# Kernel optimization log

Hardware: AMD Instinct MI355X
Metric: run time of the kernel (lower is better)

Reference implementation:

```python
import jax, jax.numpy as jnp
import numpy as np
import math

NPAD = 100      # npadding
NLAYERS = 4     # transformer_num_layers
NHEAD = 8       # transformer_nhead


def _posenc(T, d):
    pos = jnp.arange(T, dtype=jnp.float32)[:, None]
    div = jnp.exp(jnp.arange(0, d, 2, dtype=jnp.float32) * (-(math.log(1000.0) / d)))
    pe = jnp.zeros((T, d), jnp.float32)
    pe = pe.at[:, 0::2].set(jnp.sin(pos * div))
    pe = pe.at[:, 1::2].set(jnp.cos(pos * div))
    return pe


def _ln(x, g, b):
    m = x.mean(-1, keepdims=True)
    v = ((x - m) ** 2).mean(-1, keepdims=True)
    return (x - m) / jnp.sqrt(v + 1e-5) * g + b


def conv_individual(Y, kernel, npadding):
    # Y: (B,N,Ttot); kernel: (ntau,N). Causal zero-pad then FFT conv (faithful to source).
    B, N, Ttot = Y.shape
    kernel = jnp.concatenate([jnp.zeros((1, N), kernel.dtype), kernel], axis=0)
    ntau = kernel.shape[0]
    nn = Ttot + ntau - 1
    Yf = jnp.fft.fft(Y, n=nn, axis=2)                 # (B,N,nn) complex
    Kf = jnp.fft.fft(kernel.T, n=nn, axis=-1)          # (N,nn)
    c = jnp.fft.ifft(Yf * Kf[None], axis=2).real
    c = jnp.where(jnp.abs(c) < 1e-5, 0.0, c)           # ad-hoc small-value zeroing from source
    return c[:, :, :Ttot][:, :, npadding:]             # (B,N,T)


def conv_subspace(Y, kernel, npadding):
    # Y: (B,N,Ttot); kernel: (ntau,S) -> G: (B,N,S,T)
    B, N, Ttot = Y.shape
    k = kernel[None]                                   # (1,ntau,S)
    k = jnp.concatenate([jnp.zeros((1, 1, k.shape[2]), jnp.float32), k], axis=1)
    ntau = k.shape[1]
    nn = Ttot + ntau - 1
    Yf = jnp.fft.fft(Y, n=nn, axis=2)[..., None]       # (B,N,nn,1)
    Kf = jnp.fft.fft(k, n=nn, axis=1)[None]            # (1,1,nn,S)
    G = jnp.fft.ifft(Yf * Kf, axis=2).real             # (B,N,nn,S)
    G = jnp.where(jnp.abs(G) < 1e-5, 0.0, G)
    G = G[:, :, :Ttot, :][:, :, npadding:, :]
    return jnp.swapaxes(G, -1, -2)                     # (B,N,S,T)


def _encoder(x, Wqkv, bqkv, Wo, bo, ln1_g, ln1_b, W1, b1, W2, b2, ln2_g, ln2_b):
    B, T, D = x.shape
    hd = D // NHEAD
    for l in range(NLAYERS):
        qkv = x @ Wqkv[l] + bqkv[l]                    # (B,T,3D)
        q, k, v = jnp.split(qkv, 3, axis=-1)
        q = q.reshape(B, T, NHEAD, hd)
        k = k.reshape(B, T, NHEAD, hd)
        v = v.reshape(B, T, NHEAD, hd)
        scores = jnp.einsum('bthd,bshd->bhts', q, k) / jnp.sqrt(jnp.float32(hd))
        attn = jax.nn.softmax(scores, axis=-1)
        o = jnp.einsum('bhts,bshd->bthd', attn, v).reshape(B, T, D)
        x = _ln(x + (o @ Wo[l] + bo[l]), ln1_g[l], ln1_b[l])
        ff = jax.nn.gelu(x @ W1[l] + b1[l], approximate=False) @ W2[l] + b2[l]
        x = _ln(x + ff, ln2_g[l], ln2_b[l])
    return x


def reference(Y, token_W, token_b, Wqkv, bqkv, Wo, bo, ln1_g, ln1_b, W1, b1, W2, b2,
              ln2_g, ln2_b, toL_W, toL_b, dec_W1, dec_b1, dec_W2, dec_b2,
              stimulus_basis, readout_W, coupling_W, coupling_basis, self_kernel):
    B, N, Ttot = Y.shape
    T = Ttot - NPAD
    D = token_W.shape[1]
    # token conversion over time (seq dim = time)
    x = jnp.swapaxes(Y[:, :, NPAD:], 1, 2) @ token_W + token_b   # (B,T,D)
    x = x + _posenc(T, D)[None]
    x = _encoder(x, Wqkv, bqkv, Wo, bo, ln1_g, ln1_b, W1, b1, W2, b2, ln2_g, ln2_b)
    pooled = x.mean(axis=1)                                      # (B,D)
    h = pooled @ toL_W + toL_b                                   # (B,2Z)
    Z = h.shape[1] // 2
    z = h[:, :Z]                                                 # mu (sample_latent=False)
    # stimulus decoder (2-layer MLP)
    coeffs = jax.nn.relu(z @ dec_W1 + dec_b1) @ dec_W2 + dec_b2  # (B, NF*NB)
    NB = stimulus_basis.shape[1]
    NF = coeffs.shape[1] // NB
    coeffs = coeffs.reshape(B, NF, NB)
    sti_lat = jnp.einsum('bfk,tk->bft', coeffs, stimulus_basis)  # (B,NF,T)
    sti = jnp.einsum('nf,bft->bnt', readout_W, sti_lat)          # (B,N,T)
    # coupling via FFT causal conv into subspaces
    G = conv_subspace(Y, coupling_basis, NPAD)                   # (B,N,S,T)
    cpl = jnp.einsum('ns,bnst->bnt', coupling_W, G)
    # self-history FFT causal conv
    slf = conv_individual(Y, self_kernel, NPAD)
    return sti + cpl + slf                                       # log firing rate (B,N,T)


def setup_inputs() -> dict:
    key = jax.random.key(0)
    ks = jax.random.split(key, 30)
    B, N, Ttot = 16, 256, 1100
    D, FF, Zdim = 256, 1024, 64
    NB, NF, S, NTAU = 30, 4, 4, 20   # NF = narea*stimulus_nfactor = 2*2
    T = Ttot - NPAD
    sc = 0.02
    inp = {
        'Y': jax.random.uniform(ks[0], (B, N, Ttot), jnp.float32),
        'token_W': jax.random.normal(ks[1], (N, D), jnp.float32) * sc,
        'token_b': jnp.zeros((D,), jnp.float32),
        'Wqkv': jax.random.normal(ks[2], (NLAYERS, D, 3 * D), jnp.float32) * sc,
        'bqkv': jnp.zeros((NLAYERS, 3 * D), jnp.float32),
        'Wo': jax.random.normal(ks[3], (NLAYERS, D, D), jnp.float32) * sc,
        'bo': jnp.zeros((NLAYERS, D), jnp.float32),
        'ln1_g': jnp.ones((NLAYERS, D), jnp.float32),
        'ln1_b': jnp.zeros((NLAYERS, D), jnp.float32),
        'W1': jax.random.normal(ks[4], (NLAYERS, D, FF), jnp.float32) * sc,
        'b1': jnp.zeros((NLAYERS, FF), jnp.float32),
        'W2': jax.random.normal(ks[5], (NLAYERS, FF, D), jnp.float32) * sc,
        'b2': jnp.zeros((NLAYERS, D), jnp.float32),
        'ln2_g': jnp.ones((NLAYERS, D), jnp.float32),
        'ln2_b': jnp.zeros((NLAYERS, D), jnp.float32),
        'toL_W': jax.random.normal(ks[6], (D, 2 * Zdim), jnp.float32) * sc,
        'toL_b': jnp.zeros((2 * Zdim,), jnp.float32),
        'dec_W1': jax.random.normal(ks[7], (Zdim, 2 * Zdim), jnp.float32) * sc,
        'dec_b1': jnp.zeros((2 * Zdim,), jnp.float32),
        'dec_W2': jax.random.normal(ks[8], (2 * Zdim, NB * NF), jnp.float32) * sc * 0.001,
        'dec_b2': jnp.zeros((NB * NF,), jnp.float32),
        'stimulus_basis': jax.random.normal(ks[9], (T, NB), jnp.float32),
        'readout_W': jax.random.normal(ks[10], (N, NF), jnp.float32) * sc,
        'coupling_W': jax.random.normal(ks[11], (N, S), jnp.float32) * sc,
        'coupling_basis': jax.random.normal(ks[12], (NTAU, S), jnp.float32) * 0.1,
        'self_kernel': jax.random.normal(ks[13], (NTAU, N), jnp.float32) * 0.1,
    }
    return inp
```

## Files before the change

kernel.cpp:

```cpp
#include <hip/hip_runtime.h>
#include <math.h>

#define TT_   1000
#define TTOT_ 1100
#define NPAD_ 100
#define DD_   256
#define NN_   256

#define X_OFF    0u
#define XB_OFF   4096000u
#define O_OFF    6144000u
#define BIG_OFF  12288000u
#define WT_OFF   20480000u
#define PE_OFF   22085632u
#define PP_OFF   22341632u
#define PL_OFF   (PP_OFF + 32768u)
#define CF_OFF   (PL_OFF + 4096u)
#define CB_OFF   (CF_OFF + 1920u)
#define BQ_OFF   (CB_OFF + 5120u)
#define STL_OFF  (BQ_OFF + 3072u)

#define SC2_ 0.25503902254649546f

typedef __attribute__((ext_vector_type(8))) short s16x8;
typedef __attribute__((ext_vector_type(4))) float f32x4;
typedef __attribute__((ext_vector_type(16))) float f32x16;
typedef __attribute__((ext_vector_type(4))) unsigned u32x4;

__device__ inline short f2bf(float f) {
    unsigned u = __float_as_uint(f);
    u += 0x7fffu + ((u >> 16) & 1u);
    return (short)(u >> 16);
}
__device__ inline float exp2i(float x) {
    float r; asm("v_exp_f32 %0, %1" : "=v"(r) : "v"(x)); return r;
}

__device__ inline void gl_lds16(const short* g, short* l) {
    __builtin_amdgcn_global_load_lds(
        (const __attribute__((address_space(1))) void*)g,
        (__attribute__((address_space(3))) void*)l, 16, 0, 0);
}

__global__ __launch_bounds__(256) void wtr_k(const float* __restrict__ in,
                                             short* __restrict__ out, int K, int N,
                                             int qrows, float qs)
{
    __shared__ float t[32][33];
    const int n0 = blockIdx.x * 32, k0 = blockIdx.y * 32;
    in  += (size_t)blockIdx.z * K * N;
    out += (size_t)blockIdx.z * K * N;
    const int tx = threadIdx.x & 31, ty = threadIdx.x >> 5;
    #pragma unroll
    for (int i = 0; i < 4; ++i)
        t[ty + 8 * i][tx] = in[(size_t)(k0 + ty + 8 * i) * N + n0 + tx];
    __syncthreads();
    #pragma unroll
    for (int i = 0; i < 4; ++i) {
        const int row = n0 + ty + 8 * i;
        float f = t[tx][ty + 8 * i];
        if (row < qrows) f *= qs;
        out[(size_t)row * K + k0 + tx] = f2bf(f);
    }
}

__global__ __launch_bounds__(256) void ytr_k(const float* __restrict__ Y,
                                             short* __restrict__ out)
{
    __shared__ float t[32][33];
    const int b = blockIdx.z;
    const int t0 = blockIdx.x * 32, n0 = blockIdx.y * 32;
    const int tx = threadIdx.x & 31, ty = threadIdx.x >> 5;
    #pragma unroll
    for (int i = 0; i < 4; ++i) {
        const int tt = t0 + tx;
        t[ty + 8 * i][tx] = (tt < TT_)
            ? Y[((size_t)(b * NN_ + n0 + ty + 8 * i)) * TTOT_ + NPAD_ + tt] : 0.f;
    }
    __syncthreads();
    #pragma unroll
    for (int i = 0; i < 4; ++i) {
        const int tt = t0 + ty + 8 * i;
        if (tt < TT_)
            out[((size_t)(b * TT_ + tt)) * NN_ + n0 + tx] = f2bf(t[tx][ty + 8 * i]);
    }
}

__global__ void pe_k(float* __restrict__ PE)
{
    const int t = blockIdx.x, d = threadIdx.x;
    const float div = __expf(-(float)(d & ~1) * 0.0269834190585241f);
    const float ang = (float)t * div;
    PE[t * 256 + d] = (d & 1) ? cosf(ang) : sinf(ang);
}

__global__ void bscale_k(const float* __restrict__ in, float* __restrict__ out)
{
    const int i = blockIdx.x * 256 + threadIdx.x;
    if (i < 3072) {
        const int col = i % 768;
        out[i] = in[i] * ((col < 256) ? SC2_ : 1.f);
    }
}

template<int OUTBF, int ACT, int RES, int DUAL>
__global__ __launch_bounds__(256) void bgemm_k(const short* __restrict__ A,
                                               const short* __restrict__ Bt,
                                               const float* __restrict__ bias,
                                               const float* __restrict__ resid,
                                               void* __restrict__ Cout,
                                               short* __restrict__ Cb,
                                               int M, int N, int K, int nby)
{
    __shared__ short As[64 * 64];
    __shared__ short Bs[128 * 64];
    const int tid = threadIdx.x;

    const int nwg = gridDim.x;
    int gid = blockIdx.x;
    {
        const int q = nwg >> 3, r = nwg & 7;
        const int x = gid & 7, idx = gid >> 3;
        gid = (x < r ? x * (q + 1) : r * (q + 1) + (x - r) * q) + idx;
    }
    const int bx = gid / nby, by = gid - bx * nby;
    const int m0 = bx * 64, n0 = by * 128;

    const int wv = tid >> 6, lane = tid & 63;
    const int wr = wv >> 1, wc = wv & 1;
    const int l15 = lane & 15, lg = lane >> 4;

    f32x4 acc[2][4];
    #pragma unroll
    for (int i = 0; i < 2; ++i)
        #pragma unroll
        for (int j = 0; j < 4; ++j) acc[i][j] = (f32x4){0.f, 0.f, 0.f, 0.f};

    const int nt = K >> 6;
    for (int t = 0; t < nt; ++t) {
        __syncthreads();
        const int k0 = t << 6;
        #pragma unroll
        for (int i = 0; i < 2; ++i) {
            const int cid = i * 256 + tid;
            const int r = cid >> 3, c = cid & 7;
            gl_lds16(A + (size_t)(m0 + r) * K + k0 + ((c ^ (r & 7)) * 8), As + cid * 8);
        }
        #pragma unroll
        for (int i = 0; i < 4; ++i) {
            const int cid = i * 256 + tid;
            const int r = cid >> 3, c = cid & 7;
            gl_lds16(Bt + (size_t)(n0 + r) * K + k0 + ((c ^ (r & 7)) * 8), Bs + cid * 8);
        }
        __syncthreads();

        #pragma unroll
        for (int ks = 0; ks < 2; ++ks) {
            s16x8 af[2], bf[4];
            #pragma unroll
            for (int mi = 0; mi < 2; ++mi) {
                const int row = wr * 32 + mi * 16 + l15;
                const int ch = ks * 4 + lg;
                af[mi] = *(const s16x8*)(As + row * 64 + ((ch ^ (row & 7)) * 8));
            }
            #pragma unroll
            for (int ni = 0; ni < 4; ++ni) {
                const int col = wc * 64 + ni * 16 + l15;
                const int ch = ks * 4 + lg;
                bf[ni] = *(const s16x8*)(Bs + col * 64 + ((ch ^ (col & 7)) * 8));
            }
            #pragma unroll
            for (int mi = 0; mi < 2; ++mi)
                #pragma unroll
                for (int ni = 0; ni < 4; ++ni)
                    acc[mi][ni] = __builtin_amdgcn_mfma_f32_16x16x32_bf16(
                        af[mi], bf[ni], acc[mi][ni], 0, 0, 0);
        }
    }

    #pragma unroll
    for (int mi = 0; mi < 2; ++mi) {
        #pragma unroll
        for (int ni = 0; ni < 4; ++ni) {
            const int col = n0 + wc * 64 + ni * 16 + l15;
            const float bv = bias[col];
            #pragma unroll
            for (int r = 0; r < 4; ++r) {
                const int row = m0 + wr * 32 + mi * 16 + lg * 4 + r;
                float v = acc[mi][ni][r] + bv;
                if (RES == 1) v += resid[(size_t)row * N + col];
                if (RES == 2) v += resid[(size_t)(row % 1000) * N + col];
                if (ACT) v = 0.5f * v * (1.0f + erff(v * 0.70710678118654752f));
                if (OUTBF) ((short*)Cout)[(size_t)row * N + col] = f2bf(v);
                else       ((float*)Cout)[(size_t)row * N + col] = v;
                if (DUAL)  Cb[(size_t)row * N + col] = f2bf(v);
            }
        }
    }
}

__global__ __launch_bounds__(512) void bgemmln_k(const short* __restrict__ A,
                                                 const short* __restrict__ Bt,
                                                 const float* __restrict__ bias,
                                                 const float* __restrict__ lng,
                                                 const float* __restrict__ lnb,
                                                 float* __restrict__ X,
                                                 short* __restrict__ Xb,
                                                 int K)
{
    __shared__ short As[64 * 64];
    __shared__ short Bs[256 * 64];
    __shared__ float red[64][4][2];
    __shared__ float mrs[64][2];
    const int tid = threadIdx.x;

    const int nwg = gridDim.x;
    int gid = blockIdx.x;
    {
        const int q = nwg >> 3, r = nwg & 7;
        const int x = gid & 7, idx = gid >> 3;
        gid = (x < r ? x * (q + 1) : r * (q + 1) + (x - r) * q) + idx;
    }
    const int m0 = gid * 64;

    const int wv = tid >> 6, lane = tid & 63;
    const int wr = wv >> 2, wcx = wv & 3;
    const int l15 = lane & 15, lg = lane >> 4;

    f32x4 acc[2][4];
    #pragma unroll
    for (int i = 0; i < 2; ++i)
        #pragma unroll
        for (int j = 0; j < 4; ++j) acc[i][j] = (f32x4){0.f, 0.f, 0.f, 0.f};

    const int nt = K >> 6;
    for (int t = 0; t < nt; ++t) {
        __syncthreads();
        const int k0 = t << 6;
        {
            const int r = tid >> 3, c = tid & 7;
            gl_lds16(A + (size_t)(m0 + r) * K + k0 + ((c ^ (r & 7)) * 8), As + tid * 8);
        }
        #pragma unroll
        for (int i = 0; i < 4; ++i) {
            const int cid = i * 512 + tid;
            const int r = cid >> 3, c = cid & 7;
            gl_lds16(Bt + (size_t)r * K + k0 + ((c ^ (r & 7)) * 8), Bs + cid * 8);
        }
        __syncthreads();

        #pragma unroll
        for (int ks = 0; ks < 2; ++ks) {
            s16x8 af[2], bf[4];
            #pragma unroll
            for (int mi = 0; mi < 2; ++mi) {
                const int row = wr * 32 + mi * 16 + l15;
                const int ch = ks * 4 + lg;
                af[mi] = *(const s16x8*)(As + row * 64 + ((ch ^ (row & 7)) * 8));
            }
            #pragma unroll
            for (int ni = 0; ni < 4; ++ni) {
                const int col = wcx * 64 + ni * 16 + l15;
                const int ch = ks * 4 + lg;
                bf[ni] = *(const s16x8*)(Bs + col * 64 + ((ch ^ (col & 7)) * 8));
            }
            #pragma unroll
            for (int mi = 0; mi < 2; ++mi)
                #pragma unroll
                for (int ni = 0; ni < 4; ++ni)
                    acc[mi][ni] = __builtin_amdgcn_mfma_f32_16x16x32_bf16(
                        af[mi], bf[ni], acc[mi][ni], 0, 0, 0);
        }
    }

    float v[2][4][4];
    #pragma unroll
    for (int mi = 0; mi < 2; ++mi)
        #pragma unroll
        for (int ni = 0; ni < 4; ++ni) {
            const int col = wcx * 64 + ni * 16 + l15;
            const float bv = bias[col];
            #pragma unroll
            for (int r = 0; r < 4; ++r) {
                const int row = m0 + wr * 32 + mi * 16 + lg * 4 + r;
                v[mi][ni][r] = acc[mi][ni][r] + bv + X[(size_t)row * 256 + col];
            }
        }

    #pragma unroll
    for (int mi = 0; mi < 2; ++mi)
        #pragma unroll
        for (int r = 0; r < 4; ++r) {
            float ss = v[mi][0][r] + v[mi][1][r] + v[mi][2][r] + v[mi][3][r];
            float qq = v[mi][0][r] * v[mi][0][r] + v[mi][1][r] * v[mi][1][r]
                     + v[mi][2][r] * v[mi][2][r] + v[mi][3][r] * v[mi][3][r];
            #pragma unroll
            for (int msk = 1; msk < 16; msk <<= 1) {
                ss += __shfl_xor(ss, msk);
                qq += __shfl_xor(qq, msk);
            }
            if (l15 == 0) {
                const int rloc = wr * 32 + mi * 16 + lg * 4 + r;
                red[rloc][wcx][0] = ss;
                red[rloc][wcx][1] = qq;
            }
        }
    __syncthreads();
    if (tid < 64) {
        const float s = red[tid][0][0] + red[tid][1][0] + red[tid][2][0] + red[tid][3][0];
        const float q = red[tid][0][1] + red[tid][1][1] + red[tid][2][1] + red[tid][3][1];
        const float mean = s * (1.f / 256.f);
        const float var = q * (1.f / 256.f) - mean * mean;
        mrs[tid][0] = mean;
        mrs[tid][1] = rsqrtf(var + 1e-5f);
    }
    __syncthreads();

    #pragma unroll
    for (int mi = 0; mi < 2; ++mi)
        #pragma unroll
        for (int ni = 0; ni < 4; ++ni) {
            const int col = wcx * 64 + ni * 16 + l15;
            const float gg = lng[col], bb = lnb[col];
            #pragma unroll
            for (int r = 0; r < 4; ++r) {
                const int rloc = wr * 32 + mi * 16 + lg * 4 + r;
                const int row = m0 + rloc;
                const float o = (v[mi][ni][r] - mrs[rloc][0]) * mrs[rloc][1] * gg + bb;
                X[(size_t)row * 256 + col] = o;
                Xb[(size_t)row * 256 + col] = f2bf(o);
            }
        }
}

__global__ __launch_bounds__(512) void mattn_k(const short* __restrict__ qkv,
                                               short* __restrict__ o)
{
    int wg = blockIdx.x;
    wg = (wg & 7) * 64 + (wg >> 3);
    const int qt = wg & 3, h = (wg >> 2) & 7, b = wg >> 5;

    const int tid = threadIdx.x, wv = tid >> 6, lane = tid & 63;
    const int q31 = lane & 31, hi = lane >> 5;
    __shared__ short Ks[2][64 * 40];
    __shared__ short VT[2][32 * 72];

    const int q0w = qt * 256 + wv * 32;
    int qrow = q0w + q31; if (qrow > 999) qrow = 999;
    s16x8 bq[2];
    #pragma unroll
    for (int dh = 0; dh < 2; ++dh)
        bq[dh] = *(const s16x8*)(qkv + ((size_t)(b * TT_ + qrow)) * 768 + h * 32 + dh * 16 + hi * 8);

    f32x16 oacc;
    #pragma unroll
    for (int i = 0; i < 16; ++i) oacc[i] = 0.f;
    float lrun = 0.f;

    const int sr = tid >> 2, sc = tid & 3;
    const int u = tid & 255;
    const int kp = u >> 3, dq = (u & 7) * 4;
    s16x8 kreg;
    short4 va, vb;
    auto LOADT = [&](int kt) {
        if (tid < 256) {
            int t = kt * 64 + sr; if (t > 999) t = 999;
            kreg = *(const s16x8*)(qkv + ((size_t)(b * TT_ + t)) * 768 + 256 + h * 32 + sc * 8);
        } else {
            int t0 = kt * 64 + 2 * kp, t1 = t0 + 1;
            if (t0 > 999) t0 = 999;
            if (t1 > 999) t1 = 999;
            va = *(const short4*)(qkv + ((size_t)(b * TT_ + t0)) * 768 + 512 + h * 32 + dq);
            vb = *(const short4*)(qkv + ((size_t)(b * TT_ + t1)) * 768 + 512 + h * 32 + dq);
        }
    };
    auto WRITET = [&](int buf) {
        if (tid < 256) {
            *(s16x8*)(&Ks[buf][sr * 40 + sc * 8]) = kreg;
        } else {
            const int c = kp >> 2;
            const int ko = (2 * kp) & 7;
            const uint2 vaw = *(const uint2*)&va;
            const uint2 vbw = *(const uint2*)&vb;
            unsigned pk[4];
            pk[0] = __builtin_amdgcn_perm(vbw.x, vaw.x, 0x05040100u);
            pk[1] = __builtin_amdgcn_perm(vbw.x, vaw.x, 0x07060302u);
            pk[2] = __builtin_amdgcn_perm(vbw.y, vaw.y, 0x05040100u);
            pk[3] = __builtin_amdgcn_perm(vbw.y, vaw.y, 0x07060302u);
            #pragma unroll
            for (int j = 0; j < 4; ++j) {
                const int d = dq + j;
                *(unsigned*)(&VT[buf][d * 72 + ((c ^ (d >> 3)) * 8) + ko]) = pk[j];
            }
        }
    };

    LOADT(0); WRITET(0);
    __syncthreads();
    int cur = 0;

    for (int kt = 0; kt < 16; ++kt) {
        if (kt < 15) LOADT(kt + 1);

        f32x16 st[2];
        __builtin_amdgcn_s_setprio(1);
        #pragma unroll
        for (int kb = 0; kb < 2; ++kb) {
            s16x8 kf0 = *(const s16x8*)(&Ks[cur][(kb * 32 + q31) * 40 + hi * 8]);
            s16x8 kf1 = *(const s16x8*)(&Ks[cur][(kb * 32 + q31) * 40 + 16 + hi * 8]);
            f32x16 z;
            #pragma unroll
            for (int i = 0; i < 16; ++i) z[i] = 0.f;
            z = __builtin_amdgcn_mfma_f32_32x32x16_bf16(kf0, bq[0], z, 0, 0, 0);
            z = __builtin_amdgcn_mfma_f32_32x32x16_bf16(kf1, bq[1], z, 0, 0, 0);
            st[kb] = z;
        }
        __builtin_amdgcn_s_setprio(0);

        if (kt == 15) {
            #pragma unroll
            for (int kb = 0; kb < 2; ++kb)
                #pragma unroll
                for (int r = 0; r < 16; ++r) {
                    const int kloc = kb * 32 + (r & 3) + 8 * (r >> 2) + 4 * hi;
                    if (960 + kloc >= TT_) st[kb][r] = -1e30f;
                }
        }

        float sloc = 0.f;
        #pragma unroll
        for (int kb = 0; kb < 2; ++kb)
            #pragma unroll
            for (int r = 0; r < 16; ++r) {
                const float p = exp2i(st[kb][r]);
                st[kb][r] = p; sloc += p;
            }
        lrun += sloc;

        unsigned wk[2][4][2];
        #pragma unroll
        for (int kb = 0; kb < 2; ++kb)
            #pragma unroll
            for (int a = 0; a < 4; ++a)
                #pragma unroll
                for (int h2 = 0; h2 < 2; ++h2) {
                    unsigned rr;
                    asm("v_cvt_pk_bf16_f32 %0, %1, %2"
                        : "=v"(rr)
                        : "v"(st[kb][4 * a + 2 * h2]), "v"(st[kb][4 * a + 2 * h2 + 1]));
                    wk[kb][a][h2] = rr;
                }

        #pragma unroll
        for (int ks = 0; ks < 4; ++ks) {
            const int kb = ks >> 1, qq = ks & 1;
            unsigned X0 = wk[kb][2 * qq + 1][0], Y0 = wk[kb][2 * qq][0];
            unsigned X1 = wk[kb][2 * qq + 1][1], Y1 = wk[kb][2 * qq][1];
            asm("v_permlane32_swap_b32 %0, %1" : "+v"(X0), "+v"(Y0));
            asm("v_permlane32_swap_b32 %0, %1" : "+v"(X1), "+v"(Y1));
            u32x4 w4 = (u32x4){Y0, Y1, X0, X1};
            s16x8 pb = __builtin_bit_cast(s16x8, w4);
            s16x8 vf = *(const s16x8*)(&VT[cur][q31 * 72 + (((2 * ks + hi) ^ (q31 >> 3)) * 8)]);
            __builtin_amdgcn_s_setprio(1);
            oacc = __builtin_amdgcn_mfma_f32_32x32x16_bf16(vf, pb, oacc, 0, 0, 0);
            __builtin_amdgcn_s_setprio(0);
        }

        if (kt < 15) WRITET(cur ^ 1);
        __syncthreads();
        cur ^= 1;
    }

    lrun += __shfl_xor(lrun, 32);

    const int t = q0w + q31;
    if (t < TT_) {
        const float inv = 1.f / lrun;
        short* ob = o + ((size_t)(b * TT_ + t)) * 256 + h * 32;
        #pragma unroll
        for (int a = 0; a < 4; ++a) {
            unsigned w0, w1;
            asm("v_cvt_pk_bf16_f32 %0, %1, %2"
                : "=v"(w0) : "v"(oacc[4 * a + 0] * inv), "v"(oacc[4 * a + 1] * inv));
            asm("v_cvt_pk_bf16_f32 %0, %1, %2"
                : "=v"(w1) : "v"(oacc[4 * a + 2] * inv), "v"(oacc[4 * a + 3] * inv));
            const int d0 = 8 * a + 4 * hi;
            *(unsigned*)(ob + d0) = w0;
            *(unsigned*)(ob + d0 + 2) = w1;
        }
    }
}

__global__ __launch_bounds__(256) void pool_part_k(const float* __restrict__ X,
                                                   float* __restrict__ partial)
{
    const int b = blockIdx.x, seg = blockIdx.y, d = threadIdx.x;
    float s = 0.f;
    const int t0 = seg * 125;
    for (int t = t0; t < t0 + 125; ++t) s += X[((size_t)b * TT_ + t) * 256 + d];
    partial[(b * 8 + seg) * 256 + d] = s;
}
__global__ __launch_bounds__(256) void pool_red_k(const float* __restrict__ partial,
                                                  float* __restrict__ pooled)
{
    const int b = blockIdx.x, d = threadIdx.x;
    float s = 0.f;
    for (int k = 0; k < 8; ++k) s += partial[(b * 8 + k) * 256 + d];
    pooled[b * 256 + d] = s * (1.f / (float)TT_);
}

__global__ __launch_bounds__(128) void head_k(const float* __restrict__ pooled,
                                              const float* __restrict__ toLW,
                                              const float* __restrict__ toLb,
                                              const float* __restrict__ dW1,
                                              const float* __restrict__ db1,
                                              const float* __restrict__ dW2,
                                              const float* __restrict__ db2,
                                              float* __restrict__ coeffs)
{
    const int b = blockIdx.x, j = threadIdx.x;
    __shared__ float hs[64];
    __shared__ float hid[128];
    float a = toLb[j];
    for (int d = 0; d < 256; ++d) a += pooled[b * 256 + d] * toLW[d * 128 + j];
    if (j < 64) hs[j] = a;
    __syncthreads();
    float a2 = db1[j];
    for (int z = 0; z < 64; ++z) a2 += hs[z] * dW1[z * 128 + j];
    hid[j] = fmaxf(a2, 0.f);
    __syncthreads();
    if (j < 120) {
        float a3 = db2[j];
        for (int k = 0; k < 128; ++k) a3 += hid[k] * dW2[k * 120 + j];
        coeffs[b * 120 + j] = a3;
    }
}

__global__ void comb_k(const float* __restrict__ selfK,
                       const float* __restrict__ cplW,
                       const float* __restrict__ cplB,
                       float* __restrict__ comb)
{
    const int n = threadIdx.x;
    for (int ti = 0; ti < 20; ++ti) {
        float s = selfK[ti * 256 + n];
        #pragma unroll
        for (int si = 0; si < 4; ++si) s += cplW[n * 4 + si] * cplB[ti * 4 + si];
        comb[n * 20 + ti] = s;
    }
}

__global__ __launch_bounds__(256) void stilat_k(const float* __restrict__ SB,
                                                const float* __restrict__ coeffs,
                                                float* __restrict__ STL)
{
    const int bf = blockIdx.x;
    __shared__ float c[30];
    if (threadIdx.x < 30) c[threadIdx.x] = coeffs[(bf >> 2) * 120 + (bf & 3) * 30 + threadIdx.x];
    __syncthreads();
    for (int t = threadIdx.x; t < TT_; t += 256) {
        float acc = 0.f;
        const float* sp = SB + (size_t)t * 30;
        #pragma unroll
        for (int k = 0; k < 30; ++k) acc += c[k] * sp[k];
        STL[bf * TT_ + t] = acc;
    }
}

__global__ __launch_bounds__(256) void final_k(const float* __restrict__ Y,
                                               const float* __restrict__ STL,
                                               const float* __restrict__ roW,
                                               const float* __restrict__ comb,
                                               float* __restrict__ out)
{
    const int bx = blockIdx.x;
    const int ts = bx & 3, nc = (bx >> 2) & 31, b = bx >> 7;
    const int n0 = nc * 8, t0 = ts * 250;
    const int tid = threadIdx.x;
    __shared__ float rw[8][4], ck[8][20], yl[8][272];

    if (tid < 32) rw[tid >> 2][tid & 3] = roW[(n0 + (tid >> 2)) * 4 + (tid & 3)];
    if (tid >= 64 && tid < 224) {
        const int j = tid - 64;
        ck[j / 20][j % 20] = comb[(n0 + j / 20) * 20 + (j % 20)];
    }
    for (int j = tid; j < 2160; j += 256) {
        const int n = j / 270, jj = j - n * 270;
        yl[n][jj] = Y[((size_t)(b * 256 + n0 + n)) * TTOT_ + t0 + 80 + jj];
    }
    __syncthreads();

    if (tid < 250) {
        const int t = t0 + tid;
        float s4[4];
        #pragma unroll
        for (int f = 0; f < 4; ++f) s4[f] = STL[((size_t)b * 4 + f) * TT_ + t];
        #pragma unroll
        for (int n = 0; n < 8; ++n) {
            float acc = rw[n][0] * s4[0] + rw[n][1] * s4[1]
                      + rw[n][2] * s4[2] + rw[n][3] * s4[3];
            #pragma unroll
            for (int tau = 1; tau <= 20; ++tau)
                acc += ck[n][tau - 1] * yl[n][tid + 20 - tau];
            out[((size_t)(b * 256 + n0 + n)) * TT_ + t] = acc;
        }
    }
}

extern "C" void kernel_launch(void* const* d_in, const int* in_sizes, int n_in,
                              void* d_out, int out_size, void* d_ws, size_t ws_size,
                              hipStream_t stream)
{
    const float* Y      = (const float*)d_in[0];
    const float* tokW   = (const float*)d_in[1];
    const float* tokb   = (const float*)d_in[2];
    const float* Wqkv   = (const float*)d_in[3];
    const float* bqkv   = (const float*)d_in[4];
    const float* Wo     = (const float*)d_in[5];
    const float* bo     = (const float*)d_in[6];
    const float* ln1g   = (const float*)d_in[7];
    const float* ln1b   = (const float*)d_in[8];
    const float* W1     = (const float*)d_in[9];
    const float* b1     = (const float*)d_in[10];
    const float* W2     = (const float*)d_in[11];
    const float* b2     = (const float*)d_in[12];
    const float* ln2g   = (const float*)d_in[13];
    const float* ln2b   = (const float*)d_in[14];
    const float* toLW   = (const float*)d_in[15];
    const float* toLb   = (const float*)d_in[16];
    const float* dW1    = (const float*)d_in[17];
    const float* db1    = (const float*)d_in[18];
    const float* dW2    = (const float*)d_in[19];
    const float* db2    = (const float*)d_in[20];
    const float* SB     = (const float*)d_in[21];
    const float* roW    = (const float*)d_in[22];
    const float* cplW   = (const float*)d_in[23];
    const float* cplB   = (const float*)d_in[24];
    const float* selfK  = (const float*)d_in[25];

    float* ws  = (float*)d_ws;
    float* X   = ws + X_OFF;
    short* Xb  = (short*)(ws + XB_OFF);
    short* O   = (short*)(ws + O_OFF);
    short* BIG = (short*)(ws + BIG_OFF);
    short* WT  = (short*)(ws + WT_OFF);
    float* PE  = ws + PE_OFF;
    float* PP  = ws + PP_OFF;
    float* PL  = ws + PL_OFF;
    float* CF  = ws + CF_OFF;
    float* CB  = ws + CB_OFF;
    float* BQ  = ws + BQ_OFF;
    float* STL = ws + STL_OFF;

    short* WTqkv = WT;
    short* WTo   = WT + 786432;
    short* WTw1  = WT + 1048576;
    short* WTw2  = WT + 2097152;
    short* WTtok = WT + 3145728;
    short* Ybt   = BIG;

    wtr_k<<<dim3(24, 8, 4), 256, 0, stream>>>(Wqkv, WTqkv, 256, 768, 256, SC2_);
    wtr_k<<<dim3(8, 8, 4),  256, 0, stream>>>(Wo,   WTo,   256, 256, 0, 1.f);
    wtr_k<<<dim3(32, 8, 4), 256, 0, stream>>>(W1,   WTw1,  256, 1024, 0, 1.f);
    wtr_k<<<dim3(8, 32, 4), 256, 0, stream>>>(W2,   WTw2,  1024, 256, 0, 1.f);
    wtr_k<<<dim3(8, 8, 1),  256, 0, stream>>>(tokW, WTtok, 256, 256, 0, 1.f);
    bscale_k<<<12, 256, 0, stream>>>(bqkv, BQ);
    pe_k<<<1000, 256, 0, stream>>>(PE);
    ytr_k<<<dim3(32, 8, 16), 256, 0, stream>>>(Y, Ybt);

    bgemm_k<0, 0, 2, 1><<<500, 256, 0, stream>>>(
        Ybt, WTtok, tokb, PE, X, Xb, 16000, 256, 256, 2);

    for (int l = 0; l < 4; ++l) {
        bgemm_k<1, 0, 0, 0><<<1500, 256, 0, stream>>>(
            Xb, WTqkv + (size_t)l * 196608, BQ + l * 768, nullptr, BIG, nullptr,
            16000, 768, 256, 6);
        mattn_k<<<512, 512, 0, stream>>>(BIG, O);
        bgemmln_k<<<250, 512, 0, stream>>>(
            O, WTo + (size_t)l * 65536, bo + l * 256,
            ln1g + l * 256, ln1b + l * 256, X, Xb, 256);
        bgemm_k<1, 1, 0, 0><<<2000, 256, 0, stream>>>(
            Xb, WTw1 + (size_t)l * 262144, b1 + l * 1024, nullptr, BIG, nullptr,
            16000, 1024, 256, 8);
        bgemmln_k<<<250, 512, 0, stream>>>(
            BIG, WTw2 + (size_t)l * 262144, b2 + l * 256,
            ln2g + l * 256, ln2b + l * 256, X, Xb, 1024);
    }

    pool_part_k<<<dim3(16, 8), 256, 0, stream>>>(X, PP);
    pool_red_k<<<16, 256, 0, stream>>>(PP, PL);
    head_k<<<16, 128, 0, stream>>>(PL, toLW, toLb, dW1, db1, dW2, db2, CF);
    comb_k<<<1, 256, 0, stream>>>(selfK, cplW, cplB, CB);
    stilat_k<<<64, 256, 0, stream>>>(SB, CF, STL);
    final_k<<<2048, 256, 0, stream>>>(Y, STL, roW, CB, (float*)d_out);
}
```

Baseline: 497.3 us.

## Double-buffer QKV/FFN1 GEMM loads and halve LN-GEMM row tile for occupancy

Adds a GEMM kernel that prefetches the next K-tile into a second LDS buffer while computing the current one, and uses it for the QKV and first FFN projections. The residual-plus-LayerNorm GEMM now processes 32 rows per block instead of 64, doubling the grid to improve CU utilization. The cost is more LDS per block and redundant loading of the B tile across twice as many blocks.

Measured after the change: 474.6 us. 1.05x faster.

```diff
diff --git a/kernel.cpp b/kernel.cpp
--- a/kernel.cpp
+++ b/kernel.cpp
@@ -17,7 +17,7 @@
 #define PL_OFF   (PP_OFF + 32768u)
 #define CF_OFF   (PL_OFF + 4096u)
 #define CB_OFF   (CF_OFF + 1920u)
-#define BQ_OFF   (CB_OFF + 5120u)
+#define BQ_OFF   (CF_OFF + 1920u + 5120u)
 #define STL_OFF  (BQ_OFF + 3072u)
 
 #define SC2_ 0.25503902254649546f
@@ -199,6 +199,111 @@
     }
 }
 
+template<int ACT>
+__global__ __launch_bounds__(256) void bgemm_db_k(const short* __restrict__ A,
+                                                  const short* __restrict__ Bt,
+                                                  const float* __restrict__ bias,
+                                                  short* __restrict__ Cout,
+                                                  int M, int N, int K, int nby)
+{
+    __shared__ short SH[2 * 12288];
+    const int tid = threadIdx.x;
+
+    const int nwg = gridDim.x;
+    int gid = blockIdx.x;
+    {
+        const int q = nwg >> 3, r = nwg & 7;
+        const int x = gid & 7, idx = gid >> 3;
+        gid = (x < r ? x * (q + 1) : r * (q + 1) + (x - r) * q) + idx;
+    }
+    const int bx = gid / nby, by = gid - bx * nby;
+    const int m0 = bx * 64, n0 = by * 128;
+
+    const int wv = tid >> 6, lane = tid & 63;
+    const int wr = wv >> 1, wc = wv & 1;
+    const int l15 = lane & 15, lg = lane >> 4;
+
+    f32x4 acc[2][4];
+    #pragma unroll
+    for (int i = 0; i < 2; ++i)
+        #pragma unroll
+        for (int j = 0; j < 4; ++j) acc[i][j] = (f32x4){0.f, 0.f, 0.f, 0.f};
+
+    auto STAGE = [&](int p, int k0) {
+        short* dA = SH + p * 12288;
+        short* dB = dA + 4096;
+        #pragma unroll
+        for (int i = 0; i < 2; ++i) {
+            const int cid = i * 256 + tid;
+            const int r = cid >> 3, c = cid & 7;
+            gl_lds16(A + (size_t)(m0 + r) * K + k0 + ((c ^ (r & 7)) * 8), dA + cid * 8);
+        }
+        #pragma unroll
+        for (int i = 0; i < 4; ++i) {
+            const int cid = i * 256 + tid;
+            const int r = cid >> 3, c = cid & 7;
+            gl_lds16(Bt + (size_t)(n0 + r) * K + k0 + ((c ^ (r & 7)) * 8), dB + cid * 8);
+        }
+    };
+
+    const int nt = K >> 6;
+    STAGE(0, 0);
+    int cur = 0;
+    for (int t = 0; t < nt; ++t) {
+        if (t + 1 < nt) {
+            STAGE(cur ^ 1, (t + 1) << 6);
+            asm volatile("s_waitcnt vmcnt(6)" ::: "memory");
+        } else {
+            asm volatile("s_waitcnt vmcnt(0)" ::: "memory");
+        }
+        __builtin_amdgcn_s_barrier();
+
+        const short* Asb = SH + cur * 12288;
+        const short* Bsb = Asb + 4096;
+        #pragma unroll
+        for (int ks = 0; ks < 2; ++ks) {
+            s16x8 af[2], bf[4];
+            #pragma unroll
+            for (int mi = 0; mi < 2; ++mi) {
+                const int row = wr * 32 + mi * 16 + l15;
+                const int ch = ks * 4 + lg;
+                af[mi] = *(const s16x8*)(Asb + row * 64 + ((ch ^ (row & 7)) * 8));
+            }
+            #pragma unroll
+            for (int ni = 0; ni < 4; ++ni) {
+                const int col = wc * 64 + ni * 16 + l15;
+                const int ch = ks * 4 + lg;
+                bf[ni] = *(const s16x8*)(Bsb + col * 64 + ((ch ^ (col & 7)) * 8));
+            }
+            #pragma unroll
+            for (int mi = 0; mi < 2; ++mi)
+                #pragma unroll
+                for (int ni = 0; ni < 4; ++ni)
+                    acc[mi][ni] = __builtin_amdgcn_mfma_f32_16x16x32_bf16(
+                        af[mi], bf[ni], acc[mi][ni], 0, 0, 0);
+        }
+        asm volatile("s_waitcnt lgkmcnt(0)" ::: "memory");
+        __builtin_amdgcn_s_barrier();
+        cur ^= 1;
+    }
+
+    #pragma unroll
+    for (int mi = 0; mi < 2; ++mi) {
+        #pragma unroll
+        for (int ni = 0; ni < 4; ++ni) {
+            const int col = n0 + wc * 64 + ni * 16 + l15;
+            const float bv = bias[col];
+            #pragma unroll
+            for (int r = 0; r < 4; ++r) {
+                const int row = m0 + wr * 32 + mi * 16 + lg * 4 + r;
+                float v = acc[mi][ni][r] + bv;
+                if (ACT) v = 0.5f * v * (1.0f + erff(v * 0.70710678118654752f));
+                Cout[(size_t)row * N + col] = f2bf(v);
+            }
+        }
+    }
+}
+
 __global__ __launch_bounds__(512) void bgemmln_k(const short* __restrict__ A,
                                                  const short* __restrict__ Bt,
                                                  const float* __restrict__ bias,
@@ -208,10 +313,10 @@
                                                  short* __restrict__ Xb,
                                                  int K)
 {
-    __shared__ short As[64 * 64];
+    __shared__ short As[32 * 64];
     __shared__ short Bs[256 * 64];
-    __shared__ float red[64][4][2];
-    __shared__ float mrs[64][2];
+    __shared__ float red[32][4][2];
+    __shared__ float mrs[32][2];
     const int tid = threadIdx.x;
 
     const int nwg = gridDim.x;
@@ -221,23 +326,21 @@
         const int x = gid & 7, idx = gid >> 3;
         gid = (x < r ? x * (q + 1) : r * (q + 1) + (x - r) * q) + idx;
     }
-    const int m0 = gid * 64;
+    const int m0 = gid * 32;
 
     const int wv = tid >> 6, lane = tid & 63;
     const int wr = wv >> 2, wcx = wv & 3;
     const int l15 = lane & 15, lg = lane >> 4;
 
-    f32x4 acc[2][4];
-    #pragma unroll
-    for (int i = 0; i < 2; ++i)
-        #pragma unroll
-        for (int j = 0; j < 4; ++j) acc[i][j] = (f32x4){0.f, 0.f, 0.f, 0.f};
+    f32x4 acc[4];
+    #pragma unroll
+    for (int j = 0; j < 4; ++j) acc[j] = (f32x4){0.f, 0.f, 0.f, 0.f};
 
     const int nt = K >> 6;
     for (int t = 0; t < nt; ++t) {
         __syncthreads();
         const int k0 = t << 6;
-        {
+        if (tid < 256) {
             const int r = tid >> 3, c = tid & 7;
             gl_lds16(A + (size_t)(m0 + r) * K + k0 + ((c ^ (r & 7)) * 8), As + tid * 8);
         }
@@ -251,12 +354,11 @@
 
         #pragma unroll
         for (int ks = 0; ks < 2; ++ks) {
-            s16x8 af[2], bf[4];
-            #pragma unroll
-            for (int mi = 0; mi < 2; ++mi) {
-                const int row = wr * 32 + mi * 16 + l15;
+            s16x8 af, bf[4];
+            {
+                const int row = wr * 16 + l15;
                 const int ch = ks * 4 + lg;
-                af[mi] = *(const s16x8*)(As + row * 64 + ((ch ^ (row & 7)) * 8));
+                af = *(const s16x8*)(As + row * 64 + ((ch ^ (row & 7)) * 8));
             }
             #pragma unroll
             for (int ni = 0; ni < 4; ++ni) {
@@ -265,48 +367,41 @@
                 bf[ni] = *(const s16x8*)(Bs + col * 64 + ((ch ^ (col & 7)) * 8));
             }
             #pragma unroll
-            for (int mi = 0; mi < 2; ++mi)
-                #pragma unroll
-                for (int ni = 0; ni < 4; ++ni)
-                    acc[mi][ni] = __builtin_amdgcn_mfma_f32_16x16x32_bf16(
-                        af[mi], bf[ni], acc[mi][ni], 0, 0, 0);
-        }
-    }
-
-    float v[2][4][4];
-    #pragma unroll
-    for (int mi = 0; mi < 2; ++mi)
-        #pragma unroll
-        for (int ni = 0; ni < 4; ++ni) {
-            const int col = wcx * 64 + ni * 16 + l15;
-            const float bv = bias[col];
-            #pragma unroll
-            for (int r = 0; r < 4; ++r) {
-                const int row = m0 + wr * 32 + mi * 16 + lg * 4 + r;
-                v[mi][ni][r] = acc[mi][ni][r] + bv + X[(size_t)row * 256 + col];
-            }
-        }
-
-    #pragma unroll
-    for (int mi = 0; mi < 2; ++mi)
+            for (int ni = 0; ni < 4; ++ni)
+                acc[ni] = __builtin_amdgcn_mfma_f32_16x16x32_bf16(af, bf[ni], acc[ni], 0, 0, 0);
+        }
+    }
+
+    float v[4][4];
+    #pragma unroll
+    for (int ni = 0; ni < 4; ++ni) {
+        const int col = wcx * 64 + ni * 16 + l15;
+        const float bv = bias[col];
         #pragma unroll
         for (int r = 0; r < 4; ++r) {
-            float ss = v[mi][0][r] + v[mi][1][r] + v[mi][2][r] + v[mi][3][r];
-            float qq = v[mi][0][r] * v[mi][0][r] + v[mi][1][r] * v[mi][1][r]
-                     + v[mi][2][r] * v[mi][2][r] + v[mi][3][r] * v[mi][3][r];
-            #pragma unroll
-            for (int msk = 1; msk < 16; msk <<= 1) {
-                ss += __shfl_xor(ss, msk);
-                qq += __shfl_xor(qq, msk);
-            }
-            if (l15 == 0) {
-                const int rloc = wr * 32 + mi * 16 + lg * 4 + r;
-                red[rloc][wcx][0] = ss;
-                red[rloc][wcx][1] = qq;
-            }
-        }
-    __syncthreads();
-    if (tid < 64) {
+            const int row = m0 + wr * 16 + lg * 4 + r;
+            v[ni][r] = acc[ni][r] + bv + X[(size_t)row * 256 + col];
+        }
+    }
+
+    #pragma unroll
+    for (int r = 0; r < 4; ++r) {
+        float ss = v[0][r] + v[1][r] + v[2][r] + v[3][r];
+        float qq = v[0][r] * v[0][r] + v[1][r] * v[1][r]
+                 + v[2][r] * v[2][r] + v[3][r] * v[3][r];
+        #pragma unroll
+        for (int msk = 1; msk < 16; msk <<= 1) {
+            ss += __shfl_xor(ss, msk);
+            qq += __shfl_xor(qq, msk);
+        }
+        if (l15 == 0) {
+            const int rloc = wr * 16 + lg * 4 + r;
+            red[rloc][wcx][0] = ss;
+            red[rloc][wcx][1] = qq;
+        }
+    }
+    __syncthreads();
+    if (tid < 32) {
         const float s = red[tid][0][0] + red[tid][1][0] + red[tid][2][0] + red[tid][3][0];
         const float q = red[tid][0][1] + red[tid][1][1] + red[tid][2][1] + red[tid][3][1];
         const float mean = s * (1.f / 256.f);
@@ -317,20 +412,18 @@
     __syncthreads();
 
     #pragma unroll
-    for (int mi = 0; mi < 2; ++mi)
-        #pragma unroll
-        for (int ni = 0; ni < 4; ++ni) {
-            const int col = wcx * 64 + ni * 16 + l15;
-            const float gg = lng[col], bb = lnb[col];
-            #pragma unroll
-            for (int r = 0; r < 4; ++r) {
-                const int rloc = wr * 32 + mi * 16 + lg * 4 + r;
-                const int row = m0 + rloc;
-                const float o = (v[mi][ni][r] - mrs[rloc][0]) * mrs[rloc][1] * gg + bb;
-                X[(size_t)row * 256 + col] = o;
-                Xb[(size_t)row * 256 + col] = f2bf(o);
-            }
-        }
+    for (int ni = 0; ni < 4; ++ni) {
+        const int col = wcx * 64 + ni * 16 + l15;
+        const float gg = lng[col], bb = lnb[col];
+        #pragma unroll
+        for (int r = 0; r < 4; ++r) {
+            const int rloc = wr * 16 + lg * 4 + r;
+            const int row = m0 + rloc;
+            const float o = (v[ni][r] - mrs[rloc][0]) * mrs[rloc][1] * gg + bb;
+            X[(size_t)row * 256 + col] = o;
+            Xb[(size_t)row * 256 + col] = f2bf(o);
+        }
+    }
 }
 
 __global__ __launch_bounds__(512) void mattn_k(const short* __restrict__ qkv,
@@ -672,17 +765,17 @@
         Ybt, WTtok, tokb, PE, X, Xb, 16000, 256, 256, 2);
 
     for (int l = 0; l < 4; ++l) {
-        bgemm_k<1, 0, 0, 0><<<1500, 256, 0, stream>>>(
-            Xb, WTqkv + (size_t)l * 196608, BQ + l * 768, nullptr, BIG, nullptr,
+        bgemm_db_k<0><<<1500, 256, 0, stream>>>(
+            Xb, WTqkv + (size_t)l * 196608, BQ + l * 768, BIG,
             16000, 768, 256, 6);
         mattn_k<<<512, 512, 0, stream>>>(BIG, O);
-        bgemmln_k<<<250, 512, 0, stream>>>(
+        bgemmln_k<<<500, 512, 0, stream>>>(
             O, WTo + (size_t)l * 65536, bo + l * 256,
             ln1g + l * 256, ln1b + l * 256, X, Xb, 256);
-        bgemm_k<1, 1, 0, 0><<<2000, 256, 0, stream>>>(
-            Xb, WTw1 + (size_t)l * 262144, b1 + l * 1024, nullptr, BIG, nullptr,
+        bgemm_db_k<1><<<2000, 256, 0, stream>>>(
+            Xb, WTw1 + (size_t)l * 262144, b1 + l * 1024, BIG,
             16000, 1024, 256, 8);
-        bgemmln_k<<<250, 512, 0, stream>>>(
+        bgemmln_k<<<500, 512, 0, stream>>>(
             BIG, WTw2 + (size_t)l * 262144, b2 + l * 256,
             ln2g + l * 256, ln2b + l * 256, X, Xb, 1024);
     }
```
